# Kernel tuning notes

Hardware: AMD Instinct MI355X
Metric: run time of the kernel (lower is better)

The kernel has to match this reference:

```python
import jax, jax.numpy as jnp
import numpy as np

B, S, D, H, PD = 64, 256, 256, 8, 8
HD = D // H          # 32 head dim
P8 = D // 8          # 32 pos feature dim


def setup_inputs() -> dict:
    key = jax.random.key(0)
    ks = jax.random.split(key, 14)
    n = lambda k, shp, s=0.05: jax.random.normal(k, shp, dtype=jnp.float32) * s
    return {
        "x": jax.random.normal(ks[0], (B, S, D), dtype=jnp.float32),
        "pos": jax.random.normal(ks[1], (B, S, PD), dtype=jnp.float32),
        "Wq": n(ks[2], (D, D)),                 # torch Linear convention [out, in]
        "Wk": n(ks[3], (D, D)),
        "pos_w1": n(ks[4], (PD, PD)),
        "pos_b1": n(ks[5], (PD,)),
        "pos_w2": n(ks[6], (P8, PD)),
        "pos_b2": n(ks[7], (P8,)),
        "head_w": n(ks[8], (H, P8)),
        "head_b": n(ks[9], (H,)),
        "gate": jnp.ones((H,), dtype=jnp.float32),
        "v_embed": n(ks[10], (D * D,), 1.0 / np.sqrt(D)),  # new_embeds param
        "out_w": n(ks[11], (D, D)),
        "out_b": n(ks[12], (D,)),
    }


def reference(x, pos, Wq, Wk, pos_w1, pos_b1, pos_w2, pos_b2,
              head_w, head_b, gate, v_embed, out_w, out_b):
    b, s, d = x.shape
    h = gate.shape[0]
    hd = d // h
    # QKV projections -> [B, H, S, hd]
    q = (x @ Wq.T).reshape(b, s, h, hd).transpose(0, 2, 1, 3)
    k = (x @ Wk.T).reshape(b, s, h, hd).transpose(0, 2, 1, 3)
    v = (x @ v_embed.reshape(d, d).T).reshape(b, s, h, hd).transpose(0, 2, 1, 3)
    # standard QK softmax attention [B, H, S, S]
    scale = 1.0 / jnp.sqrt(jnp.asarray(hd, x.dtype))
    attn = jax.nn.softmax(jnp.einsum('bhsd,bhtd->bhst', q, k) * scale, axis=-1)
    # relative-position attention: MLP on pos, broadcast pairwise diff, per-head score
    p = jax.nn.relu(pos @ pos_w1.T + pos_b1) @ pos_w2.T + pos_b2      # [B, S, D//8]
    diff = p[:, :, None, :] - p[:, None, :, :]                          # [B, S, S, D//8]
    pos_scores = jnp.einsum('bstc,hc->bhst', diff, head_w) + head_b[None, :, None, None]
    pos_attn = jax.nn.softmax(pos_scores, axis=-1)
    # gate, blend, renormalize
    g = jax.nn.sigmoid(gate)[None, :, None, None]
    a = (1.0 - g) * attn + g * pos_attn
    a = a / a.sum(axis=-1, keepdims=True)
    # output (dropout rate = 0 -> identity)
    out = jnp.einsum('bhst,bhtd->bshd', a, v).reshape(b, s, d)
    return out @ out_w.T + out_b
```

## Files before the change

### kernel.cpp

```cpp
#include <hip/hip_runtime.h>
#include <math.h>

#define BB 64
#define SS 256
#define DD 256
#define HH 8
#define HDIM 32
#define MROWS (BB*SS)

typedef unsigned short u16;
typedef unsigned int u32;
typedef _Float16 f16;
typedef __attribute__((ext_vector_type(8))) _Float16 half8;
typedef __attribute__((ext_vector_type(16))) float f32x16;

union U4H8 { uint4 u; half8 h; };

__device__ __forceinline__ u16 f16b(float a) {
    f16 h = (f16)a; return __builtin_bit_cast(u16, h);
}
__device__ __forceinline__ u32 pk_rne(float a, float b) {
    return (u32)f16b(a) | ((u32)f16b(b) << 16);
}
__device__ __forceinline__ void pksplit2(float a, float b, u32& hw, u32& lw) {
    auto h = __builtin_amdgcn_cvt_pkrtz(a, b);
    hw = __builtin_bit_cast(u32, h);
    auto l = __builtin_amdgcn_cvt_pkrtz(a - (float)h[0], b - (float)h[1]);
    lw = __builtin_bit_cast(u32, l);
}
__device__ __forceinline__ void split8f(const float* e, uint4& h4, uint4& l4) {
    pksplit2(e[0], e[1], h4.x, l4.x);
    pksplit2(e[2], e[3], h4.y, l4.y);
    pksplit2(e[4], e[5], h4.z, l4.z);
    pksplit2(e[6], e[7], h4.w, l4.w);
}
__device__ __forceinline__ f32x16 mfma16f(half8 a, half8 b, f32x16 c) {
    return __builtin_amdgcn_mfma_f32_32x32x16_f16(a, b, c, 0, 0, 0);
}

__global__ __launch_bounds__(256)
void wconv(const float* __restrict__ Wq, const float* __restrict__ Wk,
           const float* __restrict__ Wv, const float* __restrict__ Wo,
           u16* __restrict__ WH) {
    const int bx = blockIdx.x;
    const int sel = bx >> 6;
    const float* src = (sel == 0) ? Wq : (sel == 1) ? Wk : (sel == 2) ? Wv : Wo;
    const int i = (bx & 63) * 1024 + threadIdx.x * 4;
    float4 v = *reinterpret_cast<const float4*>(src + i);
    *reinterpret_cast<uint2*>(WH + (size_t)sel * 65536 + i) =
        make_uint2(pk_rne(v.x, v.y), pk_rne(v.z, v.w));
}

template<bool QKV>
__global__ __launch_bounds__(256, 3)
void gemm_mfma(const float* __restrict__ A, const u16* __restrict__ WH,
               const float* __restrict__ bias,
               float* __restrict__ C0, float* __restrict__ C1,
               float* __restrict__ C2, int wbase) {
    __shared__ u16 Ah[128*40], Al[128*40];

    const int tid = threadIdx.x;
    const int lane = tid & 63, wv = tid >> 6;
    const int wm = wv >> 1, wn = wv & 1;
    const int hh = lane >> 5, ln = lane & 31;
    const int bx = blockIdx.x, m0 = blockIdx.y * 128;

    float* C; int n0, nstack0;
    if (QKV) {
        const int sel = bx >> 1;
        C = (sel == 0) ? C0 : (sel == 1) ? C1 : C2;
        n0 = (bx & 1) * 128;
        nstack0 = bx * 128;
    } else {
        C = C0; n0 = bx * 128; nstack0 = wbase + bx * 128;
    }

    f32x16 acc[2][2];
    #pragma unroll
    for (int i = 0; i < 2; i++)
        #pragma unroll
        for (int j = 0; j < 2; j++)
            #pragma unroll
            for (int r = 0; r < 16; r++) acc[i][j][r] = 0.f;

    const int g0 = tid, g1 = 256 + tid;
    const int r0 = g0 >> 2, c80 = g0 & 3;
    const int r1 = g1 >> 2, c81 = g1 & 3;
    const float* pA0 = A + (size_t)(m0 + r0) * 256 + c80 * 8;
    const float* pA1 = A + (size_t)(m0 + r1) * 256 + c81 * 8;

    const u16* WHrow = WH + (size_t)(nstack0 + wn*64 + ln) * 256;

    float4 fa0 = *reinterpret_cast<const float4*>(pA0);
    float4 fb0 = *reinterpret_cast<const float4*>(pA0 + 4);
    float4 fa1 = *reinterpret_cast<const float4*>(pA1);
    float4 fb1 = *reinterpret_cast<const float4*>(pA1 + 4);

    #pragma unroll
    for (int s = 0; s < 8; s++) {
        const int kb = s * 32;
        {
            uint4 h4, l4;
            float e0[8] = {fa0.x,fa0.y,fa0.z,fa0.w,fb0.x,fb0.y,fb0.z,fb0.w};
            split8f(e0, h4, l4);
            *reinterpret_cast<uint4*>(&Ah[r0*40 + c80*8]) = h4;
            *reinterpret_cast<uint4*>(&Al[r0*40 + c80*8]) = l4;
            float e1[8] = {fa1.x,fa1.y,fa1.z,fa1.w,fb1.x,fb1.y,fb1.z,fb1.w};
            split8f(e1, h4, l4);
            *reinterpret_cast<uint4*>(&Ah[r1*40 + c81*8]) = h4;
            *reinterpret_cast<uint4*>(&Al[r1*40 + c81*8]) = l4;
        }
        __syncthreads();
        if (s < 7) {
            fa0 = *reinterpret_cast<const float4*>(pA0 + kb + 32);
            fb0 = *reinterpret_cast<const float4*>(pA0 + kb + 36);
            fa1 = *reinterpret_cast<const float4*>(pA1 + kb + 32);
            fb1 = *reinterpret_cast<const float4*>(pA1 + kb + 36);
        }

        U4H8 wf[2][2];
        #pragma unroll
        for (int tn = 0; tn < 2; tn++)
            #pragma unroll
            for (int ks = 0; ks < 2; ks++)
                wf[tn][ks].u = *reinterpret_cast<const uint4*>(
                    WHrow + (size_t)tn*32*256 + kb + ks*16 + hh*8);
        U4H8 afh[2][2], afl[2][2];
        #pragma unroll
        for (int tm = 0; tm < 2; tm++)
            #pragma unroll
            for (int ks = 0; ks < 2; ks++) {
                const int el = (wm*64 + tm*32 + ln)*40 + ks*16 + hh*8;
                afh[tm][ks].u = *reinterpret_cast<const uint4*>(&Ah[el]);
                afl[tm][ks].u = *reinterpret_cast<const uint4*>(&Al[el]);
            }
        #pragma unroll
        for (int tm = 0; tm < 2; tm++)
            #pragma unroll
            for (int tn = 0; tn < 2; tn++)
                #pragma unroll
                for (int ks = 0; ks < 2; ks++) {
                    acc[tm][tn] = mfma16f(afh[tm][ks].h, wf[tn][ks].h, acc[tm][tn]);
                    acc[tm][tn] = mfma16f(afl[tm][ks].h, wf[tn][ks].h, acc[tm][tn]);
                }
        __syncthreads();
    }

    #pragma unroll
    for (int tm = 0; tm < 2; tm++)
        #pragma unroll
        for (int tn = 0; tn < 2; tn++) {
            float bv = 0.f;
            if (!QKV) bv = bias[n0 + wn*64 + tn*32 + ln];
            #pragma unroll
            for (int r = 0; r < 16; r++) {
                const int mm = m0 + wm*64 + tm*32 + (r&3) + 8*(r>>2) + 4*hh;
                C[(size_t)mm*256 + n0 + wn*64 + tn*32 + ln] = acc[tm][tn][r] + bv;
            }
        }
}

__global__ __launch_bounds__(256)
void pos_kernel(const float* __restrict__ pos, const float* __restrict__ w1,
                const float* __restrict__ b1, const float* __restrict__ w2,
                const float* __restrict__ b2, const float* __restrict__ hw,
                float* __restrict__ E) {
    __shared__ float sw1[64], sb1[8], sw2[256], sb2[32], shw[256];
    const int tid = threadIdx.x;
    if (tid < 64)  sw1[tid] = w1[tid];
    if (tid < 8)   sb1[tid] = b1[tid];
    sw2[tid] = w2[tid];
    if (tid < 32)  sb2[tid] = b2[tid];
    shw[tid] = hw[tid];
    __syncthreads();

    const int row = blockIdx.x * 256 + tid;
    float pv[8];
    float4 p0 = *reinterpret_cast<const float4*>(pos + (size_t)row * 8);
    float4 p1 = *reinterpret_cast<const float4*>(pos + (size_t)row * 8 + 4);
    pv[0]=p0.x; pv[1]=p0.y; pv[2]=p0.z; pv[3]=p0.w;
    pv[4]=p1.x; pv[5]=p1.y; pv[6]=p1.z; pv[7]=p1.w;

    float h1[8];
    #pragma unroll
    for (int j = 0; j < 8; j++) {
        float a = sb1[j];
        #pragma unroll
        for (int i = 0; i < 8; i++) a = fmaf(pv[i], sw1[j*8+i], a);
        h1[j] = fmaxf(a, 0.f);
    }
    float p[32];
    #pragma unroll
    for (int c = 0; c < 32; c++) {
        float a = sb2[c];
        #pragma unroll
        for (int j = 0; j < 8; j++) a = fmaf(h1[j], sw2[c*8+j], a);
        p[c] = a;
    }
    const int b = row >> 8, s = row & 255;
    #pragma unroll
    for (int h = 0; h < 8; h++) {
        float e = 0.f;
        #pragma unroll
        for (int c = 0; c < 32; c++) e = fmaf(p[c], shw[h*32+c], e);
        E[((size_t)(b*8 + h) << 8) + s] = e;
    }
}

__global__ __launch_bounds__(256, 4)
void attn_kernel(const float* __restrict__ Q, const float* __restrict__ Kb,
                 const float* __restrict__ Vb, const float* __restrict__ E,
                 const float* __restrict__ gate, float* __restrict__ O) {
    __shared__ u16 Ks[256*40];
    __shared__ u16 Vt[32*264];
    __shared__ float ws[256];
    __shared__ float red[4];
    __shared__ float pvp[8][33];
    __shared__ float pvs[32];

    const int tid = threadIdx.x;
    const int bh = blockIdx.x, b = bh >> 3, h = bh & 7;
    const size_t base = (size_t)b * SS * DD + (size_t)h * HDIM;
    const float SCALE = 0.17677669529663687f;

    {
        const int t = tid;
        const float* kr = Kb + base + (size_t)t * DD;
        const float* vr = Vb + base + (size_t)t * DD;
        float kx[32], vx[32];
        #pragma unroll
        for (int i = 0; i < 8; i++) {
            float4 kv = *reinterpret_cast<const float4*>(kr + i*4);
            float4 vv = *reinterpret_cast<const float4*>(vr + i*4);
            kx[i*4+0]=kv.x; kx[i*4+1]=kv.y; kx[i*4+2]=kv.z; kx[i*4+3]=kv.w;
            vx[i*4+0]=vv.x; vx[i*4+1]=vv.y; vx[i*4+2]=vv.z; vx[i*4+3]=vv.w;
        }
        #pragma unroll
        for (int c = 0; c < 4; c++) {
            uint4 w;
            w.x = pk_rne(kx[c*8+0], kx[c*8+1]);
            w.y = pk_rne(kx[c*8+2], kx[c*8+3]);
            w.z = pk_rne(kx[c*8+4], kx[c*8+5]);
            w.w = pk_rne(kx[c*8+6], kx[c*8+7]);
            *reinterpret_cast<uint4*>(&Ks[t*40 + c*8]) = w;
        }
        #pragma unroll
        for (int d = 0; d < 32; d++) Vt[d*264 + t] = f16b(vx[d]);

        float w = __expf(-E[((size_t)bh << 8) + t]);
        ws[t] = w;
        float v = w;
        #pragma unroll
        for (int off = 32; off > 0; off >>= 1) v += __shfl_down(v, off);
        if ((tid & 63) == 0) red[tid >> 6] = v;
    }
    __syncthreads();
    const float psum = red[0] + red[1] + red[2] + red[3];

    {
        int d = tid & 31, ch = tid >> 5;
        float acc = 0.f;
        #pragma unroll
        for (int tb = 0; tb < 4; tb++) {
            U4H8 hv;
            hv.u = *reinterpret_cast<const uint4*>(&Vt[d*264 + ch*32 + tb*8]);
            #pragma unroll
            for (int j = 0; j < 8; j++)
                acc = fmaf(ws[ch*32 + tb*8 + j], (float)hv.h[j], acc);
        }
        pvp[ch][d] = acc;
    }
    __syncthreads();
    if (tid < 32) {
        float s = 0.f;
        #pragma unroll
        for (int i = 0; i < 8; i++) s += pvp[i][tid];
        pvs[tid] = s;
    }
    __syncthreads();

    const int lane = tid & 63, wv = tid >> 6;
    const int hh2 = lane >> 5, lq = lane & 31;
    const float g = 1.f / (1.f + __expf(-gate[h]));
    const float c2 = g / psum;

    #pragma unroll
    for (int qi = 0; qi < 2; qi++) {
        const int q0 = (wv * 2 + qi) * 32;
        U4H8 qh[2], ql[2];
        const float* qrow = Q + base + (size_t)(q0 + lq) * DD;
        #pragma unroll
        for (int ks = 0; ks < 2; ks++) {
            float4 a = *reinterpret_cast<const float4*>(qrow + ks*16 + hh2*8);
            float4 c = *reinterpret_cast<const float4*>(qrow + ks*16 + hh2*8 + 4);
            float e[8] = {a.x,a.y,a.z,a.w,c.x,c.y,c.z,c.w};
            split8f(e, qh[ks].u, ql[ks].u);
        }

        f32x16 acco;
        #pragma unroll
        for (int r = 0; r < 16; r++) acco[r] = 0.f;
        float rowsum = 0.f;

        #pragma unroll
        for (int tt = 0; tt < 8; tt++) {
            f32x16 accs;
            #pragma unroll
            for (int r = 0; r < 16; r++) accs[r] = 0.f;
            const int trow = tt*32 + lq;
            #pragma unroll
            for (int ks = 0; ks < 2; ks++) {
                U4H8 kf;
                kf.u = *reinterpret_cast<const uint4*>(&Ks[trow*40 + ks*16 + hh2*8]);
                accs = mfma16f(kf.h, qh[ks].h, accs);
                accs = mfma16f(kf.h, ql[ks].h, accs);
            }
            u32 PH[8], PL[8];
            #pragma unroll
            for (int j = 0; j < 8; j++) {
                float p0 = __expf(accs[2*j]   * SCALE);
                float p1 = __expf(accs[2*j+1] * SCALE);
                rowsum += p0 + p1;
                pksplit2(p0, p1, PH[j], PL[j]);
            }
            #pragma unroll
            for (int ks = 0; ks < 2; ks++) {
                u32 HA0 = PH[ks*4+0], HA1 = PH[ks*4+1];
                u32 HB0 = PH[ks*4+2], HB1 = PH[ks*4+3];
                u32 LA0 = PL[ks*4+0], LA1 = PL[ks*4+1];
                u32 LB0 = PL[ks*4+2], LB1 = PL[ks*4+3];
                u32 XA0 = (u32)__shfl_xor((int)HA0, 32);
                u32 XA1 = (u32)__shfl_xor((int)HA1, 32);
                u32 XB0 = (u32)__shfl_xor((int)HB0, 32);
                u32 XB1 = (u32)__shfl_xor((int)HB1, 32);
                u32 YA0 = (u32)__shfl_xor((int)LA0, 32);
                u32 YA1 = (u32)__shfl_xor((int)LA1, 32);
                u32 YB0 = (u32)__shfl_xor((int)LB0, 32);
                u32 YB1 = (u32)__shfl_xor((int)LB1, 32);
                U4H8 bhf, blf, vf;
                bhf.u = make_uint4(hh2 ? XB0 : HA0, hh2 ? XB1 : HA1,
                                   hh2 ? HB0 : XA0, hh2 ? HB1 : XA1);
                blf.u = make_uint4(hh2 ? YB0 : LA0, hh2 ? YB1 : LA1,
                                   hh2 ? LB0 : YA0, hh2 ? LB1 : YA1);
                vf.u = *reinterpret_cast<const uint4*>(
                    &Vt[lq*264 + tt*32 + ks*16 + hh2*8]);
                acco = mfma16f(vf.h, bhf.h, acco);
                acco = mfma16f(vf.h, blf.h, acco);
            }
        }

        rowsum += __shfl_xor(rowsum, 32);
        const float c1 = (1.f - g) / rowsum;
        float* orow = O + base + (size_t)(q0 + lq) * DD;
        #pragma unroll
        for (int r = 0; r < 16; r++) {
            int d = (r & 3) + 8*(r >> 2) + 4*hh2;
            orow[d] = c1 * acco[r] + c2 * pvs[d];
        }
    }
}

extern "C" void kernel_launch(void* const* d_in, const int* in_sizes, int n_in,
                              void* d_out, int out_size, void* d_ws, size_t ws_size,
                              hipStream_t stream) {
    const float* x    = (const float*)d_in[0];
    const float* pos  = (const float*)d_in[1];
    const float* Wq   = (const float*)d_in[2];
    const float* Wk   = (const float*)d_in[3];
    const float* pw1  = (const float*)d_in[4];
    const float* pb1  = (const float*)d_in[5];
    const float* pw2  = (const float*)d_in[6];
    const float* pb2  = (const float*)d_in[7];
    const float* hw   = (const float*)d_in[8];
    const float* gate = (const float*)d_in[10];
    const float* vemb = (const float*)d_in[11];
    const float* ow   = (const float*)d_in[12];
    const float* ob   = (const float*)d_in[13];
    float* out = (float*)d_out;

    const size_t NBS = (size_t)MROWS * DD;
    float* Qb   = (float*)d_ws;
    float* Kbuf = Qb + NBS;
    float* Vbuf = Kbuf + NBS;
    float* Ob   = Vbuf + NBS;
    float* Eb   = Ob + NBS;
    u16*  WHp  = (u16*)(Eb + 131072);

    hipLaunchKernelGGL(wconv, dim3(256), dim3(256), 0, stream,
                       Wq, Wk, vemb, ow, WHp);
    hipLaunchKernelGGL((gemm_mfma<true>), dim3(6, MROWS/128), dim3(256), 0, stream,
                       x, WHp, nullptr, Qb, Kbuf, Vbuf, 0);
    hipLaunchKernelGGL(pos_kernel, dim3(MROWS / 256), dim3(256), 0, stream,
                       pos, pw1, pb1, pw2, pb2, hw, Eb);
    hipLaunchKernelGGL(attn_kernel, dim3(BB * HH), dim3(256), 0, stream,
                       Qb, Kbuf, Vbuf, Eb, gate, Ob);
    hipLaunchKernelGGL((gemm_mfma<false>), dim3(2, MROWS/128), dim3(256), 0, stream,
                       Ob, WHp, ob, out, out, out, 768);
}
```

Baseline: 164.0 us.

## Store intermediates as split fp16 hi/lo pairs and split attention across more blocks

The pipeline now stores its intermediates as fp16 instead of fp32. A new xsplit kernel pre-splits x into fp16 hi/lo halves, and the QKV GEMM writes Q as a hi/lo pair and K and V as fp16. Attention reads these directly, uses twice as many blocks (each handles half the queries), and writes O as a hi/lo fp16 pair for the output GEMM. The position-weighted V sum moves into a separate posv kernel, and s_setprio is placed around the MFMA sections. The aim is to cut global memory traffic and in-kernel conversion work and to raise parallelism in attention, at the cost of an extra launch, an x round-trip through memory, and scattered 16-bit stores in the GEMM epilogue.

```diff
diff --git a/kernel.cpp b/kernel.cpp
--- a/kernel.cpp
+++ b/kernel.cpp
@@ -14,7 +14,7 @@
 typedef __attribute__((ext_vector_type(8))) _Float16 half8;
 typedef __attribute__((ext_vector_type(16))) float f32x16;
 
-union U4H8 { uint4 u; half8 h; };
+union U4H8 { uint4 u; half8 h; u16 s[8]; };
 
 __device__ __forceinline__ u16 f16b(float a) {
     f16 h = (f16)a; return __builtin_bit_cast(u16, h);
@@ -51,12 +51,26 @@
         make_uint2(pk_rne(v.x, v.y), pk_rne(v.z, v.w));
 }
 
-template<bool QKV>
+__global__ __launch_bounds__(256)
+void xsplit(const float* __restrict__ x, u16* __restrict__ Xh,
+            u16* __restrict__ Xl) {
+    const size_t i = ((size_t)blockIdx.x * 256 + threadIdx.x) * 8;
+    float4 a = *reinterpret_cast<const float4*>(x + i);
+    float4 b = *reinterpret_cast<const float4*>(x + i + 4);
+    float e[8] = {a.x,a.y,a.z,a.w,b.x,b.y,b.z,b.w};
+    uint4 h4, l4;
+    split8f(e, h4, l4);
+    *reinterpret_cast<uint4*>(Xh + i) = h4;
+    *reinterpret_cast<uint4*>(Xl + i) = l4;
+}
+
+template<int MODE>
 __global__ __launch_bounds__(256, 3)
-void gemm_mfma(const float* __restrict__ A, const u16* __restrict__ WH,
-               const float* __restrict__ bias,
-               float* __restrict__ C0, float* __restrict__ C1,
-               float* __restrict__ C2, int wbase) {
+void gemm_mfma(const u16* __restrict__ AH, const u16* __restrict__ AL,
+               const u16* __restrict__ WH, const float* __restrict__ bias,
+               float* __restrict__ Cf, u16* __restrict__ Ph0,
+               u16* __restrict__ Pl0, u16* __restrict__ Ph1,
+               u16* __restrict__ Ph2, int wbase) {
     __shared__ u16 Ah[128*40], Al[128*40];
 
     const int tid = threadIdx.x;
@@ -65,14 +79,13 @@
     const int hh = lane >> 5, ln = lane & 31;
     const int bx = blockIdx.x, m0 = blockIdx.y * 128;
 
-    float* C; int n0, nstack0;
-    if (QKV) {
-        const int sel = bx >> 1;
-        C = (sel == 0) ? C0 : (sel == 1) ? C1 : C2;
+    int sel = 0, n0, nstack0;
+    if (MODE == 1) {
+        sel = bx >> 1;
         n0 = (bx & 1) * 128;
         nstack0 = bx * 128;
     } else {
-        C = C0; n0 = bx * 128; nstack0 = wbase + bx * 128;
+        n0 = bx * 128; nstack0 = wbase + bx * 128;
     }
 
     f32x16 acc[2][2];
@@ -86,36 +99,31 @@
     const int g0 = tid, g1 = 256 + tid;
     const int r0 = g0 >> 2, c80 = g0 & 3;
     const int r1 = g1 >> 2, c81 = g1 & 3;
-    const float* pA0 = A + (size_t)(m0 + r0) * 256 + c80 * 8;
-    const float* pA1 = A + (size_t)(m0 + r1) * 256 + c81 * 8;
+    const u16* pH0 = AH + (size_t)(m0 + r0) * 256 + c80 * 8;
+    const u16* pL0 = AL + (size_t)(m0 + r0) * 256 + c80 * 8;
+    const u16* pH1 = AH + (size_t)(m0 + r1) * 256 + c81 * 8;
+    const u16* pL1 = AL + (size_t)(m0 + r1) * 256 + c81 * 8;
 
     const u16* WHrow = WH + (size_t)(nstack0 + wn*64 + ln) * 256;
 
-    float4 fa0 = *reinterpret_cast<const float4*>(pA0);
-    float4 fb0 = *reinterpret_cast<const float4*>(pA0 + 4);
-    float4 fa1 = *reinterpret_cast<const float4*>(pA1);
-    float4 fb1 = *reinterpret_cast<const float4*>(pA1 + 4);
+    uint4 h0 = *reinterpret_cast<const uint4*>(pH0);
+    uint4 l0 = *reinterpret_cast<const uint4*>(pL0);
+    uint4 h1 = *reinterpret_cast<const uint4*>(pH1);
+    uint4 l1 = *reinterpret_cast<const uint4*>(pL1);
 
     #pragma unroll
     for (int s = 0; s < 8; s++) {
         const int kb = s * 32;
-        {
-            uint4 h4, l4;
-            float e0[8] = {fa0.x,fa0.y,fa0.z,fa0.w,fb0.x,fb0.y,fb0.z,fb0.w};
-            split8f(e0, h4, l4);
-            *reinterpret_cast<uint4*>(&Ah[r0*40 + c80*8]) = h4;
-            *reinterpret_cast<uint4*>(&Al[r0*40 + c80*8]) = l4;
-            float e1[8] = {fa1.x,fa1.y,fa1.z,fa1.w,fb1.x,fb1.y,fb1.z,fb1.w};
-            split8f(e1, h4, l4);
-            *reinterpret_cast<uint4*>(&Ah[r1*40 + c81*8]) = h4;
-            *reinterpret_cast<uint4*>(&Al[r1*40 + c81*8]) = l4;
-        }
+        *reinterpret_cast<uint4*>(&Ah[r0*40 + c80*8]) = h0;
+        *reinterpret_cast<uint4*>(&Al[r0*40 + c80*8]) = l0;
+        *reinterpret_cast<uint4*>(&Ah[r1*40 + c81*8]) = h1;
+        *reinterpret_cast<uint4*>(&Al[r1*40 + c81*8]) = l1;
         __syncthreads();
         if (s < 7) {
-            fa0 = *reinterpret_cast<const float4*>(pA0 + kb + 32);
-            fb0 = *reinterpret_cast<const float4*>(pA0 + kb + 36);
-            fa1 = *reinterpret_cast<const float4*>(pA1 + kb + 32);
-            fb1 = *reinterpret_cast<const float4*>(pA1 + kb + 36);
+            h0 = *reinterpret_cast<const uint4*>(pH0 + kb + 32);
+            l0 = *reinterpret_cast<const uint4*>(pL0 + kb + 32);
+            h1 = *reinterpret_cast<const uint4*>(pH1 + kb + 32);
+            l1 = *reinterpret_cast<const uint4*>(pL1 + kb + 32);
         }
 
         U4H8 wf[2][2];
@@ -134,6 +142,7 @@
                 afh[tm][ks].u = *reinterpret_cast<const uint4*>(&Ah[el]);
                 afl[tm][ks].u = *reinterpret_cast<const uint4*>(&Al[el]);
             }
+        __builtin_amdgcn_s_setprio(1);
         #pragma unroll
         for (int tm = 0; tm < 2; tm++)
             #pragma unroll
@@ -143,6 +152,7 @@
                     acc[tm][tn] = mfma16f(afh[tm][ks].h, wf[tn][ks].h, acc[tm][tn]);
                     acc[tm][tn] = mfma16f(afl[tm][ks].h, wf[tn][ks].h, acc[tm][tn]);
                 }
+        __builtin_amdgcn_s_setprio(0);
         __syncthreads();
     }
 
@@ -150,12 +160,34 @@
     for (int tm = 0; tm < 2; tm++)
         #pragma unroll
         for (int tn = 0; tn < 2; tn++) {
-            float bv = 0.f;
-            if (!QKV) bv = bias[n0 + wn*64 + tn*32 + ln];
-            #pragma unroll
-            for (int r = 0; r < 16; r++) {
-                const int mm = m0 + wm*64 + tm*32 + (r&3) + 8*(r>>2) + 4*hh;
-                C[(size_t)mm*256 + n0 + wn*64 + tn*32 + ln] = acc[tm][tn][r] + bv;
+            const int col = n0 + wn*64 + tn*32 + ln;
+            const int mb = m0 + wm*64 + tm*32;
+            if (MODE == 0) {
+                const float bv = bias[col];
+                #pragma unroll
+                for (int r = 0; r < 16; r++) {
+                    const int mm = mb + (r&3) + 8*(r>>2) + 4*hh;
+                    Cf[(size_t)mm*256 + col] = acc[tm][tn][r] + bv;
+                }
+            } else if (sel == 0) {
+                #pragma unroll
+                for (int rp = 0; rp < 8; rp++) {
+                    const int r = 2*rp;
+                    const int mm = mb + (r&3) + 8*(r>>2) + 4*hh;
+                    u32 hw, lw;
+                    pksplit2(acc[tm][tn][r], acc[tm][tn][r+1], hw, lw);
+                    Ph0[(size_t)mm*256 + col]     = (u16)hw;
+                    Ph0[(size_t)(mm+1)*256 + col] = (u16)(hw >> 16);
+                    Pl0[(size_t)mm*256 + col]     = (u16)lw;
+                    Pl0[(size_t)(mm+1)*256 + col] = (u16)(lw >> 16);
+                }
+            } else {
+                u16* P = (sel == 1) ? Ph1 : Ph2;
+                #pragma unroll
+                for (int r = 0; r < 16; r++) {
+                    const int mm = mb + (r&3) + 8*(r>>2) + 4*hh;
+                    P[(size_t)mm*256 + col] = f16b(acc[tm][tn][r]);
+                }
             }
         }
 }
@@ -207,156 +239,166 @@
     }
 }
 
-__global__ __launch_bounds__(256, 4)
-void attn_kernel(const float* __restrict__ Q, const float* __restrict__ Kb,
-                 const float* __restrict__ Vb, const float* __restrict__ E,
-                 const float* __restrict__ gate, float* __restrict__ O) {
-    __shared__ u16 Ks[256*40];
-    __shared__ u16 Vt[32*264];
+__global__ __launch_bounds__(256)
+void posv(const float* __restrict__ E, const u16* __restrict__ Vh,
+          float* __restrict__ PVn) {
     __shared__ float ws[256];
     __shared__ float red[4];
     __shared__ float pvp[8][33];
-    __shared__ float pvs[32];
-
     const int tid = threadIdx.x;
     const int bh = blockIdx.x, b = bh >> 3, h = bh & 7;
-    const size_t base = (size_t)b * SS * DD + (size_t)h * HDIM;
-    const float SCALE = 0.17677669529663687f;
-
-    {
-        const int t = tid;
-        const float* kr = Kb + base + (size_t)t * DD;
-        const float* vr = Vb + base + (size_t)t * DD;
-        float kx[32], vx[32];
-        #pragma unroll
-        for (int i = 0; i < 8; i++) {
-            float4 kv = *reinterpret_cast<const float4*>(kr + i*4);
-            float4 vv = *reinterpret_cast<const float4*>(vr + i*4);
-            kx[i*4+0]=kv.x; kx[i*4+1]=kv.y; kx[i*4+2]=kv.z; kx[i*4+3]=kv.w;
-            vx[i*4+0]=vv.x; vx[i*4+1]=vv.y; vx[i*4+2]=vv.z; vx[i*4+3]=vv.w;
-        }
-        #pragma unroll
-        for (int c = 0; c < 4; c++) {
-            uint4 w;
-            w.x = pk_rne(kx[c*8+0], kx[c*8+1]);
-            w.y = pk_rne(kx[c*8+2], kx[c*8+3]);
-            w.z = pk_rne(kx[c*8+4], kx[c*8+5]);
-            w.w = pk_rne(kx[c*8+6], kx[c*8+7]);
-            *reinterpret_cast<uint4*>(&Ks[t*40 + c*8]) = w;
-        }
-        #pragma unroll
-        for (int d = 0; d < 32; d++) Vt[d*264 + t] = f16b(vx[d]);
-
-        float w = __expf(-E[((size_t)bh << 8) + t]);
-        ws[t] = w;
-        float v = w;
-        #pragma unroll
-        for (int off = 32; off > 0; off >>= 1) v += __shfl_down(v, off);
-        if ((tid & 63) == 0) red[tid >> 6] = v;
-    }
+
+    float w = __expf(-E[((size_t)bh << 8) + tid]);
+    ws[tid] = w;
+    float v = w;
+    #pragma unroll
+    for (int off = 32; off > 0; off >>= 1) v += __shfl_down(v, off);
+    if ((tid & 63) == 0) red[tid >> 6] = v;
     __syncthreads();
     const float psum = red[0] + red[1] + red[2] + red[3];
 
-    {
-        int d = tid & 31, ch = tid >> 5;
-        float acc = 0.f;
-        #pragma unroll
-        for (int tb = 0; tb < 4; tb++) {
-            U4H8 hv;
-            hv.u = *reinterpret_cast<const uint4*>(&Vt[d*264 + ch*32 + tb*8]);
-            #pragma unroll
-            for (int j = 0; j < 8; j++)
-                acc = fmaf(ws[ch*32 + tb*8 + j], (float)hv.h[j], acc);
-        }
-        pvp[ch][d] = acc;
-    }
+    const int d = tid & 31, ch = tid >> 5;
+    float acc = 0.f;
+    #pragma unroll
+    for (int i = 0; i < 32; i++) {
+        const int t = ch*32 + i;
+        f16 vv = __builtin_bit_cast(f16, Vh[(((size_t)b*256 + t) << 8) + h*32 + d]);
+        acc = fmaf(ws[t], (float)vv, acc);
+    }
+    pvp[ch][d] = acc;
     __syncthreads();
     if (tid < 32) {
         float s = 0.f;
         #pragma unroll
         for (int i = 0; i < 8; i++) s += pvp[i][tid];
-        pvs[tid] = s;
+        PVn[bh*32 + tid] = s / psum;
+    }
+}
+
+__global__ __launch_bounds__(256, 4)
+void attn_kernel(const u16* __restrict__ Qh, const u16* __restrict__ Ql,
+                 const u16* __restrict__ Kh, const u16* __restrict__ Vh,
+                 const float* __restrict__ PVn, const float* __restrict__ gate,
+                 u16* __restrict__ Oh, u16* __restrict__ Ol) {
+    __shared__ u16 Ks[256*40];
+    __shared__ u16 Vt[32*264];
+    __shared__ float sPV[32];
+
+    const int tid = threadIdx.x;
+    const int bid = blockIdx.x;
+    const int bh = bid >> 1, hb = bid & 1;
+    const int b = bh >> 3, h = bh & 7;
+    const size_t rbase = (size_t)b * 256;
+    const int cbase = h * 32;
+    const float SCALE = 0.17677669529663687f;
+
+    {
+        const int t = tid;
+        const u16* kr = Kh + ((rbase + t) << 8) + cbase;
+        const u16* vr = Vh + ((rbase + t) << 8) + cbase;
+        #pragma unroll
+        for (int c = 0; c < 4; c++)
+            *reinterpret_cast<uint4*>(&Ks[t*40 + c*8]) =
+                *reinterpret_cast<const uint4*>(kr + c*8);
+        U4H8 vv[4];
+        #pragma unroll
+        for (int c = 0; c < 4; c++)
+            vv[c].u = *reinterpret_cast<const uint4*>(vr + c*8);
+        #pragma unroll
+        for (int c = 0; c < 4; c++)
+            #pragma unroll
+            for (int j = 0; j < 8; j++)
+                Vt[(c*8+j)*264 + t] = vv[c].s[j];
+        if (tid < 32) sPV[tid] = PVn[bh*32 + tid];
     }
     __syncthreads();
 
     const int lane = tid & 63, wv = tid >> 6;
     const int hh2 = lane >> 5, lq = lane & 31;
+    const int q0 = hb*128 + wv*32;
+
+    U4H8 qh[2], ql[2];
+    {
+        const u16* qrh = Qh + ((rbase + q0 + lq) << 8) + cbase;
+        const u16* qrl = Ql + ((rbase + q0 + lq) << 8) + cbase;
+        #pragma unroll
+        for (int ks = 0; ks < 2; ks++) {
+            qh[ks].u = *reinterpret_cast<const uint4*>(qrh + ks*16 + hh2*8);
+            ql[ks].u = *reinterpret_cast<const uint4*>(qrl + ks*16 + hh2*8);
+        }
+    }
+
+    f32x16 acco;
+    #pragma unroll
+    for (int r = 0; r < 16; r++) acco[r] = 0.f;
+    float rowsum = 0.f;
+
+    #pragma unroll
+    for (int tt = 0; tt < 8; tt++) {
+        f32x16 accs;
+        #pragma unroll
+        for (int r = 0; r < 16; r++) accs[r] = 0.f;
+        const int trow = tt*32 + lq;
+        __builtin_amdgcn_s_setprio(1);
+        #pragma unroll
+        for (int ks = 0; ks < 2; ks++) {
+            U4H8 kf;
+            kf.u = *reinterpret_cast<const uint4*>(&Ks[trow*40 + ks*16 + hh2*8]);
+            accs = mfma16f(kf.h, qh[ks].h, accs);
+            accs = mfma16f(kf.h, ql[ks].h, accs);
+        }
+        __builtin_amdgcn_s_setprio(0);
+        u32 PH[8], PL[8];
+        #pragma unroll
+        for (int j = 0; j < 8; j++) {
+            float p0 = __expf(accs[2*j]   * SCALE);
+            float p1 = __expf(accs[2*j+1] * SCALE);
+            rowsum += p0 + p1;
+            pksplit2(p0, p1, PH[j], PL[j]);
+        }
+        #pragma unroll
+        for (int ks = 0; ks < 2; ks++) {
+            u32 HA0 = PH[ks*4+0], HA1 = PH[ks*4+1];
+            u32 HB0 = PH[ks*4+2], HB1 = PH[ks*4+3];
+            u32 LA0 = PL[ks*4+0], LA1 = PL[ks*4+1];
+            u32 LB0 = PL[ks*4+2], LB1 = PL[ks*4+3];
+            u32 XA0 = (u32)__shfl_xor((int)HA0, 32);
+            u32 XA1 = (u32)__shfl_xor((int)HA1, 32);
+            u32 XB0 = (u32)__shfl_xor((int)HB0, 32);
+            u32 XB1 = (u32)__shfl_xor((int)HB1, 32);
+            u32 YA0 = (u32)__shfl_xor((int)LA0, 32);
+            u32 YA1 = (u32)__shfl_xor((int)LA1, 32);
+            u32 YB0 = (u32)__shfl_xor((int)LB0, 32);
+            u32 YB1 = (u32)__shfl_xor((int)LB1, 32);
+            U4H8 bhf, blf, vf;
+            bhf.u = make_uint4(hh2 ? XB0 : HA0, hh2 ? XB1 : HA1,
+                               hh2 ? HB0 : XA0, hh2 ? HB1 : XA1);
+            blf.u = make_uint4(hh2 ? YB0 : LA0, hh2 ? YB1 : LA1,
+                               hh2 ? LB0 : YA0, hh2 ? LB1 : YA1);
+            vf.u = *reinterpret_cast<const uint4*>(
+                &Vt[lq*264 + tt*32 + ks*16 + hh2*8]);
+            __builtin_amdgcn_s_setprio(1);
+            acco = mfma16f(vf.h, bhf.h, acco);
+            acco = mfma16f(vf.h, blf.h, acco);
+            __builtin_amdgcn_s_setprio(0);
+        }
+    }
+
+    rowsum += __shfl_xor(rowsum, 32);
     const float g = 1.f / (1.f + __expf(-gate[h]));
-    const float c2 = g / psum;
-
-    #pragma unroll
-    for (int qi = 0; qi < 2; qi++) {
-        const int q0 = (wv * 2 + qi) * 32;
-        U4H8 qh[2], ql[2];
-        const float* qrow = Q + base + (size_t)(q0 + lq) * DD;
-        #pragma unroll
-        for (int ks = 0; ks < 2; ks++) {
-            float4 a = *reinterpret_cast<const float4*>(qrow + ks*16 + hh2*8);
-            float4 c = *reinterpret_cast<const float4*>(qrow + ks*16 + hh2*8 + 4);
-            float e[8] = {a.x,a.y,a.z,a.w,c.x,c.y,c.z,c.w};
-            split8f(e, qh[ks].u, ql[ks].u);
-        }
-
-        f32x16 acco;
-        #pragma unroll
-        for (int r = 0; r < 16; r++) acco[r] = 0.f;
-        float rowsum = 0.f;
-
-        #pragma unroll
-        for (int tt = 0; tt < 8; tt++) {
-            f32x16 accs;
-            #pragma unroll
-            for (int r = 0; r < 16; r++) accs[r] = 0.f;
-            const int trow = tt*32 + lq;
-            #pragma unroll
-            for (int ks = 0; ks < 2; ks++) {
-                U4H8 kf;
-                kf.u = *reinterpret_cast<const uint4*>(&Ks[trow*40 + ks*16 + hh2*8]);
-                accs = mfma16f(kf.h, qh[ks].h, accs);
-                accs = mfma16f(kf.h, ql[ks].h, accs);
-            }
-            u32 PH[8], PL[8];
-            #pragma unroll
-            for (int j = 0; j < 8; j++) {
-                float p0 = __expf(accs[2*j]   * SCALE);
-                float p1 = __expf(accs[2*j+1] * SCALE);
-                rowsum += p0 + p1;
-                pksplit2(p0, p1, PH[j], PL[j]);
-            }
-            #pragma unroll
-            for (int ks = 0; ks < 2; ks++) {
-                u32 HA0 = PH[ks*4+0], HA1 = PH[ks*4+1];
-                u32 HB0 = PH[ks*4+2], HB1 = PH[ks*4+3];
-                u32 LA0 = PL[ks*4+0], LA1 = PL[ks*4+1];
-                u32 LB0 = PL[ks*4+2], LB1 = PL[ks*4+3];
-                u32 XA0 = (u32)__shfl_xor((int)HA0, 32);
-                u32 XA1 = (u32)__shfl_xor((int)HA1, 32);
-                u32 XB0 = (u32)__shfl_xor((int)HB0, 32);
-                u32 XB1 = (u32)__shfl_xor((int)HB1, 32);
-                u32 YA0 = (u32)__shfl_xor((int)LA0, 32);
-                u32 YA1 = (u32)__shfl_xor((int)LA1, 32);
-                u32 YB0 = (u32)__shfl_xor((int)LB0, 32);
-                u32 YB1 = (u32)__shfl_xor((int)LB1, 32);
-                U4H8 bhf, blf, vf;
-                bhf.u = make_uint4(hh2 ? XB0 : HA0, hh2 ? XB1 : HA1,
-                                   hh2 ? HB0 : XA0, hh2 ? HB1 : XA1);
-                blf.u = make_uint4(hh2 ? YB0 : LA0, hh2 ? YB1 : LA1,
-                                   hh2 ? LB0 : YA0, hh2 ? LB1 : YA1);
-                vf.u = *reinterpret_cast<const uint4*>(
-                    &Vt[lq*264 + tt*32 + ks*16 + hh2*8]);
-                acco = mfma16f(vf.h, bhf.h, acco);
-                acco = mfma16f(vf.h, blf.h, acco);
-            }
-        }
-
-        rowsum += __shfl_xor(rowsum, 32);
-        const float c1 = (1.f - g) / rowsum;
-        float* orow = O + base + (size_t)(q0 + lq) * DD;
-        #pragma unroll
-        for (int r = 0; r < 16; r++) {
-            int d = (r & 3) + 8*(r >> 2) + 4*hh2;
-            orow[d] = c1 * acco[r] + c2 * pvs[d];
-        }
+    const float c1 = (1.f - g) / rowsum;
+    u16* ohp = Oh + ((rbase + q0 + lq) << 8) + cbase;
+    u16* olp = Ol + ((rbase + q0 + lq) << 8) + cbase;
+    #pragma unroll
+    for (int rp = 0; rp < 8; rp++) {
+        const int r = 2*rp;
+        const int d0 = (r & 3) + 8*(r >> 2) + 4*hh2;
+        float o0 = c1 * acco[r]   + g * sPV[d0];
+        float o1 = c1 * acco[r+1] + g * sPV[d0+1];
+        u32 hw, lw;
+        pksplit2(o0, o1, hw, lw);
+        *reinterpret_cast<u32*>(ohp + d0) = hw;
+        *reinterpret_cast<u32*>(olp + d0) = lw;
     }
 }
 
@@ -379,21 +421,30 @@
     float* out = (float*)d_out;
 
     const size_t NBS = (size_t)MROWS * DD;
-    float* Qb   = (float*)d_ws;
-    float* Kbuf = Qb + NBS;
-    float* Vbuf = Kbuf + NBS;
-    float* Ob   = Vbuf + NBS;
-    float* Eb   = Ob + NBS;
-    u16*  WHp  = (u16*)(Eb + 131072);
+    u16* Qh  = (u16*)d_ws;
+    u16* Ql  = Qh + NBS;
+    u16* Kh  = Ql + NBS;
+    u16* Vh  = Kh + NBS;
+    u16* Oh  = Vh + NBS;
+    u16* Ol  = Oh + NBS;
+    u16* Xh  = Ol + NBS;
+    u16* Xl  = Xh + NBS;
+    u16* WHp = Xl + NBS;
+    float* Eb  = (float*)(WHp + 262144);
+    float* PVn = Eb + 131072;
 
     hipLaunchKernelGGL(wconv, dim3(256), dim3(256), 0, stream,
                        Wq, Wk, vemb, ow, WHp);
-    hipLaunchKernelGGL((gemm_mfma<true>), dim3(6, MROWS/128), dim3(256), 0, stream,
-                       x, WHp, nullptr, Qb, Kbuf, Vbuf, 0);
+    hipLaunchKernelGGL(xsplit, dim3(MROWS*DD/2048), dim3(256), 0, stream,
+                       x, Xh, Xl);
     hipLaunchKernelGGL(pos_kernel, dim3(MROWS / 256), dim3(256), 0, stream,
                        pos, pw1, pb1, pw2, pb2, hw, Eb);
-    hipLaunchKernelGGL(attn_kernel, dim3(BB * HH), dim3(256), 0, stream,
-                       Qb, Kbuf, Vbuf, Eb, gate, Ob);
-    hipLaunchKernelGGL((gemm_mfma<false>), dim3(2, MROWS/128), dim3(256), 0, stream,
-                       Ob, WHp, ob, out, out, out, 768);
-}
+    hipLaunchKernelGGL((gemm_mfma<1>), dim3(6, MROWS/128), dim3(256), 0, stream,
+                       Xh, Xl, WHp, nullptr, nullptr, Qh, Ql, Kh, Vh, 0);
+    hipLaunchKernelGGL(posv, dim3(BB*HH), dim3(256), 0, stream,
+                       Eb, Vh, PVn);
+    hipLaunchKernelGGL(attn_kernel, dim3(BB*HH*2), dim3(256), 0, stream,
+                       Qh, Ql, Kh, Vh, PVn, gate, Oh, Ol);
+    hipLaunchKernelGGL((gemm_mfma<0>), dim3(2, MROWS/128), dim3(256), 0, stream,
+                       Oh, Ol, WHp, ob, out, nullptr, nullptr, nullptr, nullptr, 768);
+}
```

Result: slower. 176.6 us (+7.7%).

## Merge weight-convert and pos kernels, split attention query rows across two blocks

Applied to the files above, without the earlier changes.

Folds the weight fp16 conversion and the positional MLP into one prep launch, removing one kernel launch. The attention grid doubles so that each block handles 128 query rows of one (batch, head) instead of 256, which raises parallelism across CUs. In exchange, every block must still load the full K/V tile and compute the positional prologue, so that work is duplicated. s_setprio hints are also added around MFMA sections in the GEMM and attention kernels.

```diff
diff --git a/kernel.cpp b/kernel.cpp
--- a/kernel.cpp
+++ b/kernel.cpp
@@ -14,7 +14,7 @@
 typedef __attribute__((ext_vector_type(8))) _Float16 half8;
 typedef __attribute__((ext_vector_type(16))) float f32x16;
 
-union U4H8 { uint4 u; half8 h; };
+union U4H8 { uint4 u; half8 h; u16 s[8]; };
 
 __device__ __forceinline__ u16 f16b(float a) {
     f16 h = (f16)a; return __builtin_bit_cast(u16, h);
@@ -39,16 +39,66 @@
 }
 
 __global__ __launch_bounds__(256)
-void wconv(const float* __restrict__ Wq, const float* __restrict__ Wk,
-           const float* __restrict__ Wv, const float* __restrict__ Wo,
-           u16* __restrict__ WH) {
-    const int bx = blockIdx.x;
-    const int sel = bx >> 6;
-    const float* src = (sel == 0) ? Wq : (sel == 1) ? Wk : (sel == 2) ? Wv : Wo;
-    const int i = (bx & 63) * 1024 + threadIdx.x * 4;
-    float4 v = *reinterpret_cast<const float4*>(src + i);
-    *reinterpret_cast<uint2*>(WH + (size_t)sel * 65536 + i) =
-        make_uint2(pk_rne(v.x, v.y), pk_rne(v.z, v.w));
+void prep(const float* __restrict__ Wq, const float* __restrict__ Wk,
+          const float* __restrict__ Wv, const float* __restrict__ Wo,
+          u16* __restrict__ WH,
+          const float* __restrict__ pos, const float* __restrict__ w1,
+          const float* __restrict__ b1, const float* __restrict__ w2,
+          const float* __restrict__ b2, const float* __restrict__ hw,
+          float* __restrict__ E) {
+    __shared__ float sw1[64], sb1[8], sw2[256], sb2[32], shw[256];
+    const int tid = threadIdx.x;
+
+    if (blockIdx.x < 256) {
+        const int bx = blockIdx.x;
+        const int sel = bx >> 6;
+        const float* src = (sel == 0) ? Wq : (sel == 1) ? Wk
+                         : (sel == 2) ? Wv : Wo;
+        const int i = (bx & 63) * 1024 + tid * 4;
+        float4 v = *reinterpret_cast<const float4*>(src + i);
+        *reinterpret_cast<uint2*>(WH + (size_t)sel * 65536 + i) =
+            make_uint2(pk_rne(v.x, v.y), pk_rne(v.z, v.w));
+        return;
+    }
+
+    if (tid < 64)  sw1[tid] = w1[tid];
+    if (tid < 8)   sb1[tid] = b1[tid];
+    sw2[tid] = w2[tid];
+    if (tid < 32)  sb2[tid] = b2[tid];
+    shw[tid] = hw[tid];
+    __syncthreads();
+
+    const int row = (blockIdx.x - 256) * 256 + tid;
+    float pv[8];
+    float4 p0 = *reinterpret_cast<const float4*>(pos + (size_t)row * 8);
+    float4 p1 = *reinterpret_cast<const float4*>(pos + (size_t)row * 8 + 4);
+    pv[0]=p0.x; pv[1]=p0.y; pv[2]=p0.z; pv[3]=p0.w;
+    pv[4]=p1.x; pv[5]=p1.y; pv[6]=p1.z; pv[7]=p1.w;
+
+    float h1[8];
+    #pragma unroll
+    for (int j = 0; j < 8; j++) {
+        float a = sb1[j];
+        #pragma unroll
+        for (int i = 0; i < 8; i++) a = fmaf(pv[i], sw1[j*8+i], a);
+        h1[j] = fmaxf(a, 0.f);
+    }
+    float p[32];
+    #pragma unroll
+    for (int c = 0; c < 32; c++) {
+        float a = sb2[c];
+        #pragma unroll
+        for (int j = 0; j < 8; j++) a = fmaf(h1[j], sw2[c*8+j], a);
+        p[c] = a;
+    }
+    const int b = row >> 8, s = row & 255;
+    #pragma unroll
+    for (int h = 0; h < 8; h++) {
+        float e = 0.f;
+        #pragma unroll
+        for (int c = 0; c < 32; c++) e = fmaf(p[c], shw[h*32+c], e);
+        E[((size_t)(b*8 + h) << 8) + s] = e;
+    }
 }
 
 template<bool QKV>
@@ -134,6 +184,7 @@
                 afh[tm][ks].u = *reinterpret_cast<const uint4*>(&Ah[el]);
                 afl[tm][ks].u = *reinterpret_cast<const uint4*>(&Al[el]);
             }
+        __builtin_amdgcn_s_setprio(1);
         #pragma unroll
         for (int tm = 0; tm < 2; tm++)
             #pragma unroll
@@ -143,6 +194,7 @@
                     acc[tm][tn] = mfma16f(afh[tm][ks].h, wf[tn][ks].h, acc[tm][tn]);
                     acc[tm][tn] = mfma16f(afl[tm][ks].h, wf[tn][ks].h, acc[tm][tn]);
                 }
+        __builtin_amdgcn_s_setprio(0);
         __syncthreads();
     }
 
@@ -158,53 +210,6 @@
                 C[(size_t)mm*256 + n0 + wn*64 + tn*32 + ln] = acc[tm][tn][r] + bv;
             }
         }
-}
-
-__global__ __launch_bounds__(256)
-void pos_kernel(const float* __restrict__ pos, const float* __restrict__ w1,
-                const float* __restrict__ b1, const float* __restrict__ w2,
-                const float* __restrict__ b2, const float* __restrict__ hw,
-                float* __restrict__ E) {
-    __shared__ float sw1[64], sb1[8], sw2[256], sb2[32], shw[256];
-    const int tid = threadIdx.x;
-    if (tid < 64)  sw1[tid] = w1[tid];
-    if (tid < 8)   sb1[tid] = b1[tid];
-    sw2[tid] = w2[tid];
-    if (tid < 32)  sb2[tid] = b2[tid];
-    shw[tid] = hw[tid];
-    __syncthreads();
-
-    const int row = blockIdx.x * 256 + tid;
-    float pv[8];
-    float4 p0 = *reinterpret_cast<const float4*>(pos + (size_t)row * 8);
-    float4 p1 = *reinterpret_cast<const float4*>(pos + (size_t)row * 8 + 4);
-    pv[0]=p0.x; pv[1]=p0.y; pv[2]=p0.z; pv[3]=p0.w;
-    pv[4]=p1.x; pv[5]=p1.y; pv[6]=p1.z; pv[7]=p1.w;
-
-    float h1[8];
-    #pragma unroll
-    for (int j = 0; j < 8; j++) {
-        float a = sb1[j];
-        #pragma unroll
-        for (int i = 0; i < 8; i++) a = fmaf(pv[i], sw1[j*8+i], a);
-        h1[j] = fmaxf(a, 0.f);
-    }
-    float p[32];
-    #pragma unroll
-    for (int c = 0; c < 32; c++) {
-        float a = sb2[c];
-        #pragma unroll
-        for (int j = 0; j < 8; j++) a = fmaf(h1[j], sw2[c*8+j], a);
-        p[c] = a;
-    }
-    const int b = row >> 8, s = row & 255;
-    #pragma unroll
-    for (int h = 0; h < 8; h++) {
-        float e = 0.f;
-        #pragma unroll
-        for (int c = 0; c < 32; c++) e = fmaf(p[c], shw[h*32+c], e);
-        E[((size_t)(b*8 + h) << 8) + s] = e;
-    }
 }
 
 __global__ __launch_bounds__(256, 4)
@@ -219,7 +224,9 @@
     __shared__ float pvs[32];
 
     const int tid = threadIdx.x;
-    const int bh = blockIdx.x, b = bh >> 3, h = bh & 7;
+    const int bid = blockIdx.x;
+    const int bh = bid >> 1, hb = bid & 1;
+    const int b = bh >> 3, h = bh & 7;
     const size_t base = (size_t)b * SS * DD + (size_t)h * HDIM;
     const float SCALE = 0.17677669529663687f;
 
@@ -283,80 +290,81 @@
     const int hh2 = lane >> 5, lq = lane & 31;
     const float g = 1.f / (1.f + __expf(-gate[h]));
     const float c2 = g / psum;
-
-    #pragma unroll
-    for (int qi = 0; qi < 2; qi++) {
-        const int q0 = (wv * 2 + qi) * 32;
-        U4H8 qh[2], ql[2];
-        const float* qrow = Q + base + (size_t)(q0 + lq) * DD;
+    const int q0 = hb*128 + wv*32;
+
+    U4H8 qh[2], ql[2];
+    const float* qrow = Q + base + (size_t)(q0 + lq) * DD;
+    #pragma unroll
+    for (int ks = 0; ks < 2; ks++) {
+        float4 a = *reinterpret_cast<const float4*>(qrow + ks*16 + hh2*8);
+        float4 c = *reinterpret_cast<const float4*>(qrow + ks*16 + hh2*8 + 4);
+        float e[8] = {a.x,a.y,a.z,a.w,c.x,c.y,c.z,c.w};
+        split8f(e, qh[ks].u, ql[ks].u);
+    }
+
+    f32x16 acco;
+    #pragma unroll
+    for (int r = 0; r < 16; r++) acco[r] = 0.f;
+    float rowsum = 0.f;
+
+    #pragma unroll
+    for (int tt = 0; tt < 8; tt++) {
+        f32x16 accs;
+        #pragma unroll
+        for (int r = 0; r < 16; r++) accs[r] = 0.f;
+        const int trow = tt*32 + lq;
+        __builtin_amdgcn_s_setprio(1);
         #pragma unroll
         for (int ks = 0; ks < 2; ks++) {
-            float4 a = *reinterpret_cast<const float4*>(qrow + ks*16 + hh2*8);
-            float4 c = *reinterpret_cast<const float4*>(qrow + ks*16 + hh2*8 + 4);
-            float e[8] = {a.x,a.y,a.z,a.w,c.x,c.y,c.z,c.w};
-            split8f(e, qh[ks].u, ql[ks].u);
-        }
-
-        f32x16 acco;
-        #pragma unroll
-        for (int r = 0; r < 16; r++) acco[r] = 0.f;
-        float rowsum = 0.f;
-
-        #pragma unroll
-        for (int tt = 0; tt < 8; tt++) {
-            f32x16 accs;
-            #pragma unroll
-            for (int r = 0; r < 16; r++) accs[r] = 0.f;
-            const int trow = tt*32 + lq;
-            #pragma unroll
-            for (int ks = 0; ks < 2; ks++) {
-                U4H8 kf;
-                kf.u = *reinterpret_cast<const uint4*>(&Ks[trow*40 + ks*16 + hh2*8]);
-                accs = mfma16f(kf.h, qh[ks].h, accs);
-                accs = mfma16f(kf.h, ql[ks].h, accs);
-            }
-            u32 PH[8], PL[8];
-            #pragma unroll
-            for (int j = 0; j < 8; j++) {
-                float p0 = __expf(accs[2*j]   * SCALE);
-                float p1 = __expf(accs[2*j+1] * SCALE);
-                rowsum += p0 + p1;
-                pksplit2(p0, p1, PH[j], PL[j]);
-            }
-            #pragma unroll
-            for (int ks = 0; ks < 2; ks++) {
-                u32 HA0 = PH[ks*4+0], HA1 = PH[ks*4+1];
-                u32 HB0 = PH[ks*4+2], HB1 = PH[ks*4+3];
-                u32 LA0 = PL[ks*4+0], LA1 = PL[ks*4+1];
-                u32 LB0 = PL[ks*4+2], LB1 = PL[ks*4+3];
-                u32 XA0 = (u32)__shfl_xor((int)HA0, 32);
-                u32 XA1 = (u32)__shfl_xor((int)HA1, 32);
-                u32 XB0 = (u32)__shfl_xor((int)HB0, 32);
-                u32 XB1 = (u32)__shfl_xor((int)HB1, 32);
-                u32 YA0 = (u32)__shfl_xor((int)LA0, 32);
-                u32 YA1 = (u32)__shfl_xor((int)LA1, 32);
-                u32 YB0 = (u32)__shfl_xor((int)LB0, 32);
-                u32 YB1 = (u32)__shfl_xor((int)LB1, 32);
-                U4H8 bhf, blf, vf;
-                bhf.u = make_uint4(hh2 ? XB0 : HA0, hh2 ? XB1 : HA1,
-                                   hh2 ? HB0 : XA0, hh2 ? HB1 : XA1);
-                blf.u = make_uint4(hh2 ? YB0 : LA0, hh2 ? YB1 : LA1,
-                                   hh2 ? LB0 : YA0, hh2 ? LB1 : YA1);
-                vf.u = *reinterpret_cast<const uint4*>(
-                    &Vt[lq*264 + tt*32 + ks*16 + hh2*8]);
-                acco = mfma16f(vf.h, bhf.h, acco);
-                acco = mfma16f(vf.h, blf.h, acco);
-            }
-        }
-
-        rowsum += __shfl_xor(rowsum, 32);
-        const float c1 = (1.f - g) / rowsum;
-        float* orow = O + base + (size_t)(q0 + lq) * DD;
-        #pragma unroll
-        for (int r = 0; r < 16; r++) {
-            int d = (r & 3) + 8*(r >> 2) + 4*hh2;
-            orow[d] = c1 * acco[r] + c2 * pvs[d];
-        }
+            U4H8 kf;
+            kf.u = *reinterpret_cast<const uint4*>(&Ks[trow*40 + ks*16 + hh2*8]);
+            accs = mfma16f(kf.h, qh[ks].h, accs);
+            accs = mfma16f(kf.h, ql[ks].h, accs);
+        }
+        __builtin_amdgcn_s_setprio(0);
+        u32 PH[8], PL[8];
+        #pragma unroll
+        for (int j = 0; j < 8; j++) {
+            float p0 = __expf(accs[2*j]   * SCALE);
+            float p1 = __expf(accs[2*j+1] * SCALE);
+            rowsum += p0 + p1;
+            pksplit2(p0, p1, PH[j], PL[j]);
+        }
+        #pragma unroll
+        for (int ks = 0; ks < 2; ks++) {
+            u32 HA0 = PH[ks*4+0], HA1 = PH[ks*4+1];
+            u32 HB0 = PH[ks*4+2], HB1 = PH[ks*4+3];
+            u32 LA0 = PL[ks*4+0], LA1 = PL[ks*4+1];
+            u32 LB0 = PL[ks*4+2], LB1 = PL[ks*4+3];
+            u32 XA0 = (u32)__shfl_xor((int)HA0, 32);
+            u32 XA1 = (u32)__shfl_xor((int)HA1, 32);
+            u32 XB0 = (u32)__shfl_xor((int)HB0, 32);
+            u32 XB1 = (u32)__shfl_xor((int)HB1, 32);
+            u32 YA0 = (u32)__shfl_xor((int)LA0, 32);
+            u32 YA1 = (u32)__shfl_xor((int)LA1, 32);
+            u32 YB0 = (u32)__shfl_xor((int)LB0, 32);
+            u32 YB1 = (u32)__shfl_xor((int)LB1, 32);
+            U4H8 bhf, blf, vf;
+            bhf.u = make_uint4(hh2 ? XB0 : HA0, hh2 ? XB1 : HA1,
+                               hh2 ? HB0 : XA0, hh2 ? HB1 : XA1);
+            blf.u = make_uint4(hh2 ? YB0 : LA0, hh2 ? YB1 : LA1,
+                               hh2 ? LB0 : YA0, hh2 ? LB1 : YA1);
+            vf.u = *reinterpret_cast<const uint4*>(
+                &Vt[lq*264 + tt*32 + ks*16 + hh2*8]);
+            __builtin_amdgcn_s_setprio(1);
+            acco = mfma16f(vf.h, bhf.h, acco);
+            acco = mfma16f(vf.h, blf.h, acco);
+            __builtin_amdgcn_s_setprio(0);
+        }
+    }
+
+    rowsum += __shfl_xor(rowsum, 32);
+    const float c1 = (1.f - g) / rowsum;
+    float* orow = O + base + (size_t)(q0 + lq) * DD;
+    #pragma unroll
+    for (int r = 0; r < 16; r++) {
+        int d = (r & 3) + 8*(r >> 2) + 4*hh2;
+        orow[d] = c1 * acco[r] + c2 * pvs[d];
     }
 }
 
@@ -386,13 +394,12 @@
     float* Eb   = Ob + NBS;
     u16*  WHp  = (u16*)(Eb + 131072);
 
-    hipLaunchKernelGGL(wconv, dim3(256), dim3(256), 0, stream,
-                       Wq, Wk, vemb, ow, WHp);
+    hipLaunchKernelGGL(prep, dim3(256 + MROWS/256), dim3(256), 0, stream,
+                       Wq, Wk, vemb, ow, WHp,
+                       pos, pw1, pb1, pw2, pb2, hw, Eb);
     hipLaunchKernelGGL((gemm_mfma<true>), dim3(6, MROWS/128), dim3(256), 0, stream,
                        x, WHp, nullptr, Qb, Kbuf, Vbuf, 0);
-    hipLaunchKernelGGL(pos_kernel, dim3(MROWS / 256), dim3(256), 0, stream,
-                       pos, pw1, pb1, pw2, pb2, hw, Eb);
-    hipLaunchKernelGGL(attn_kernel, dim3(BB * HH), dim3(256), 0, stream,
+    hipLaunchKernelGGL(attn_kernel, dim3(BB*HH*2), dim3(256), 0, stream,
                        Qb, Kbuf, Vbuf, Eb, gate, Ob);
     hipLaunchKernelGGL((gemm_mfma<false>), dim3(2, MROWS/128), dim3(256), 0, stream,
                        Ob, WHp, ob, out, out, out, 768);
```

Measured after the change: 160.1 us. 2.4% less time.
